# Optimization experiments

Measured on AMD Instinct MI355X. Metric: run time of the kernel, lower is better.

The kernel has to match this reference:

```python
import jax, jax.numpy as jnp
import numpy as np

BATCH, N_SEQS, SEQ_LEN, D_IN, D_OUT = 8, 4, 2048, 512, 512
LN_EPS = 1e-5


def setup_inputs() -> dict:
    key = jax.random.key(0)
    ks = jax.random.split(key, 6)
    s_in = 1.0 / np.sqrt(D_IN)
    s_out = 1.0 / np.sqrt(D_OUT)
    return {
        "x": jax.random.normal(ks[0], (BATCH, N_SEQS * SEQ_LEN * D_IN), dtype=jnp.float32),
        "Wq": jax.random.normal(ks[1], (D_OUT, D_IN), dtype=jnp.float32) * s_in,
        "Wk": jax.random.normal(ks[2], (D_OUT, D_IN), dtype=jnp.float32) * s_in,
        "Wv": jax.random.normal(ks[3], (D_OUT, D_IN), dtype=jnp.float32) * s_in,
        "Wo": jax.random.normal(ks[4], (D_OUT, D_OUT), dtype=jnp.float32) * s_out,
        "bo": jnp.zeros((D_OUT,), dtype=jnp.float32),
        "gamma": jnp.ones((D_OUT,), dtype=jnp.float32),
        "beta": jnp.zeros((D_OUT,), dtype=jnp.float32),
    }


def _phi(x):
    # positive feature map: elu(x) + 1
    return jax.nn.elu(x) + 1.0


def reference(x, Wq, Wk, Wv, Wo, bo, gamma, beta):
    batch = x.shape[0]
    xs = x.reshape(batch * N_SEQS, SEQ_LEN, D_IN)  # [B*L, S, d_in]
    Q = _phi(jnp.einsum('bsi,oi->bso', xs, Wq))     # [B*L, S, d_out]
    K = _phi(jnp.einsum('bsi,oi->bso', xs, Wk))
    V = jnp.einsum('bsi,oi->bso', xs, Wv)
    kv = jnp.einsum('bsd,bse->bde', K, V)           # [B*L, d_out, d_out]
    num = jnp.einsum('bsd,bde->bse', Q, kv)         # [B*L, S, d_out]
    k_sum = K.sum(axis=1, keepdims=True)            # [B*L, 1, d_out]
    den = jnp.maximum((Q * k_sum).sum(axis=-1, keepdims=True), 1e-6)
    out = num / den
    y = jnp.einsum('bse,oe->bso', out, Wo) + bo + out  # out_proj + residual
    mu = y.mean(axis=-1, keepdims=True)
    var = ((y - mu) ** 2).mean(axis=-1, keepdims=True)
    y = (y - mu) * jax.lax.rsqrt(var + LN_EPS) * gamma + beta
    return y.reshape(batch, -1)
```

## Files before the change

kernel.cpp:

```cpp
#include <hip/hip_runtime.h>
#include <cstdint>

typedef __bf16 bf16x8 __attribute__((ext_vector_type(8)));
typedef float  f32x4  __attribute__((ext_vector_type(4)));

#define SEQS   32
#define SLEN   2048
#define DIM    512
#define MROWS  65536

static __device__ __forceinline__ void load_lds16(const void* g, void* l) {
  __builtin_amdgcn_global_load_lds(
      (const __attribute__((address_space(1))) void*)(uintptr_t)g,
      (__attribute__((address_space(3))) void*)(uintptr_t)l,
      16, 0, 0);
}

static __device__ __forceinline__ unsigned short bfbits(float f) {
  __bf16 h = (__bf16)f;
  unsigned short u;
  __builtin_memcpy(&u, &h, 2);
  return u;
}

static __device__ __forceinline__ void gemm_core(
    const __bf16* __restrict__ A, int lda, int arow0,
    const __bf16* __restrict__ B, int ldb, int brow0,
    int K, __bf16* Asm, __bf16* Bsm, f32x4 (&acc)[4][4])
{
  const int tid  = threadIdx.x;
  const int wave = tid >> 6;
  const int lane = tid & 63;
  const int wr = wave >> 1, wc = wave & 1;
  const int lr = lane & 15, kq = lane >> 4;

  for (int kt = 0; kt < K; kt += 64) {
#pragma unroll
    for (int q = 0; q < 4; ++q) {
      const int L  = q * 4096 + tid * 16;
      const int r  = L >> 7;
      const int sl = (L >> 4) & 7;
      const int c  = ((sl ^ (r & 7)) << 3);
      load_lds16(A + (size_t)(arow0 + r) * lda + (kt + c),
                 (char*)Asm + q * 4096 + wave * 1024);
      load_lds16(B + (size_t)(brow0 + r) * ldb + (kt + c),
                 (char*)Bsm + q * 4096 + wave * 1024);
    }
    __syncthreads();

    bf16x8 af[2][4], bfr[2][4];
#pragma unroll
    for (int kk = 0; kk < 2; ++kk)
#pragma unroll
      for (int i = 0; i < 4; ++i) {
        const int rA = wr * 64 + i * 16 + lr;
        af[kk][i] = *reinterpret_cast<const bf16x8*>(
            (char*)Asm + rA * 128 + ((((kk * 4 + kq) ^ (rA & 7))) << 4));
        const int rB = wc * 64 + i * 16 + lr;
        bfr[kk][i] = *reinterpret_cast<const bf16x8*>(
            (char*)Bsm + rB * 128 + ((((kk * 4 + kq) ^ (rB & 7))) << 4));
      }
#pragma unroll
    for (int kk = 0; kk < 2; ++kk)
#pragma unroll
      for (int i = 0; i < 4; ++i)
#pragma unroll
        for (int j = 0; j < 4; ++j)
          acc[i][j] = __builtin_amdgcn_mfma_f32_16x16x32_bf16(
              af[kk][i], bfr[kk][j], acc[i][j], 0, 0, 0);
    __syncthreads();
  }
}


__global__ __launch_bounds__(256) void cast_kernel(
    const float* __restrict__ src, __bf16* __restrict__ dst, int n8)
{
  int i = blockIdx.x * blockDim.x + threadIdx.x;
  const int stride = gridDim.x * blockDim.x;
  for (; i < n8; i += stride) {
    const float4* p = reinterpret_cast<const float4*>(src + (size_t)i * 8);
    float4 a = p[0], b2 = p[1];
    float vals[8] = {a.x, a.y, a.z, a.w, b2.x, b2.y, b2.z, b2.w};
    uint32_t w[4];
#pragma unroll
    for (int t = 0; t < 4; ++t)
      w[t] = (uint32_t)bfbits(vals[2 * t]) | ((uint32_t)bfbits(vals[2 * t + 1]) << 16);
    uint4 o; o.x = w[0]; o.y = w[1]; o.z = w[2]; o.w = w[3];
    *reinterpret_cast<uint4*>(dst + (size_t)i * 8) = o;
  }
}

__global__ __launch_bounds__(256) void cast4_kernel(
    const float* __restrict__ a, const float* __restrict__ b,
    const float* __restrict__ c, const float* __restrict__ d,
    __bf16* __restrict__ ab, __bf16* __restrict__ bb,
    __bf16* __restrict__ cb, __bf16* __restrict__ db)
{
  const int z = blockIdx.y;
  const float* src = (z == 0) ? a : (z == 1) ? b : (z == 2) ? c : d;
  __bf16* dst = (z == 0) ? ab : (z == 1) ? bb : (z == 2) ? cb : db;
  const int i = blockIdx.x * 256 + threadIdx.x;
  const float4* p = reinterpret_cast<const float4*>(src + (size_t)i * 8);
  float4 x = p[0], y = p[1];
  float vals[8] = {x.x, x.y, x.z, x.w, y.x, y.y, y.z, y.w};
  uint32_t w[4];
#pragma unroll
  for (int t = 0; t < 4; ++t)
    w[t] = (uint32_t)bfbits(vals[2 * t]) | ((uint32_t)bfbits(vals[2 * t + 1]) << 16);
  uint4 o; o.x = w[0]; o.y = w[1]; o.z = w[2]; o.w = w[3];
  *reinterpret_cast<uint4*>(dst + (size_t)i * 8) = o;
}

__global__ __launch_bounds__(512, 1) void qkv_kernel(
    const __bf16* __restrict__ xb,
    const __bf16* __restrict__ Wqb, const __bf16* __restrict__ Wkb,
    const __bf16* __restrict__ Wvb,
    __bf16* __restrict__ Q, __bf16* __restrict__ KT, __bf16* __restrict__ VT,
    float* __restrict__ ksum)
{
  __shared__ __align__(16) __bf16 As[2][256 * 64];
  __shared__ __align__(16) __bf16 Bs[2][256 * 64];
  const int b = blockIdx.x;
  const int xcd = b & 7, loc = b >> 3;
  const int brow = (loc / 6) * 8 + xcd;
  const int inner = loc % 6;
  const int z = inner >> 1, bcol = inner & 1;
  const __bf16* W = (z == 0) ? Wqb : (z == 1) ? Wkb : Wvb;

  const int tid = threadIdx.x, wave = tid >> 6, lane = tid & 63;
  const int wr = wave >> 2, wn = wave & 3;
  const int lr = lane & 15, kq = lane >> 4;

  const __bf16* Abase = xb + (size_t)(brow * 256) * DIM;
  const __bf16* Bbase = W + (size_t)(bcol * 256) * DIM;

  auto stage = [&](int s, int kt) {
#pragma unroll
    for (int q = 0; q < 4; ++q) {
      const int L  = q * 8192 + tid * 16;
      const int r  = L >> 7;
      const int sl = (L >> 4) & 7;
      const int c  = ((sl ^ (r & 7)) << 3);
      load_lds16(Abase + (size_t)r * DIM + (kt + c),
                 (char*)(&As[s][0]) + q * 8192 + wave * 1024);
      load_lds16(Bbase + (size_t)r * DIM + (kt + c),
                 (char*)(&Bs[s][0]) + q * 8192 + wave * 1024);
    }
  };

  f32x4 acc[8][4] = {};

  stage(0, 0);
  __syncthreads();
  for (int t = 0; t < 8; ++t) {
    const int cur = t & 1;
    if (t < 7) stage(cur ^ 1, (t + 1) * 64);
#pragma unroll
    for (int kk = 0; kk < 2; ++kk) {
      bf16x8 bfr[4], af[8];
#pragma unroll
      for (int j = 0; j < 4; ++j) {
        const int rB = wn * 64 + j * 16 + lr;
        bfr[j] = *reinterpret_cast<const bf16x8*>(
            (const char*)(&Bs[cur][0]) + rB * 128 + (((kk * 4 + kq) ^ (rB & 7)) << 4));
      }
#pragma unroll
      for (int i = 0; i < 8; ++i) {
        const int rA = wr * 128 + i * 16 + lr;
        af[i] = *reinterpret_cast<const bf16x8*>(
            (const char*)(&As[cur][0]) + rA * 128 + (((kk * 4 + kq) ^ (rA & 7)) << 4));
      }
#pragma unroll
      for (int i = 0; i < 8; ++i)
#pragma unroll
        for (int j = 0; j < 4; ++j)
          acc[i][j] = __builtin_amdgcn_mfma_f32_16x16x32_bf16(af[i], bfr[j], acc[i][j], 0, 0, 0);
    }
    __syncthreads();
  }

  const int m00 = brow * 256 + wr * 128 + kq * 4;
  const int n00 = bcol * 256 + wn * 64 + lr;
  if (z == 0) {
#pragma unroll
    for (int i = 0; i < 8; ++i)
#pragma unroll
      for (int j = 0; j < 4; ++j) {
        const int n = n00 + j * 16;
#pragma unroll
        for (int r = 0; r < 4; ++r) {
          const int m = m00 + i * 16 + r;
          float v = acc[i][j][r];
          v = (v > 0.f) ? (v + 1.f) : __expf(v);
          Q[(size_t)m * DIM + n] = (__bf16)v;
        }
      }
  } else {
    __bf16* T = (z == 1) ? KT : VT;
    const int seq = (brow * 256) >> 11;
    float ks[4] = {0.f, 0.f, 0.f, 0.f};
#pragma unroll
    for (int i = 0; i < 8; ++i) {
      const int mb = m00 + i * 16;
      const int s0 = mb & 2047;
#pragma unroll
      for (int j = 0; j < 4; ++j) {
        const int d = n00 + j * 16;
        unsigned short h[4];
#pragma unroll
        for (int r = 0; r < 4; ++r) {
          float v = acc[i][j][r];
          if (z == 1) { v = (v > 0.f) ? (v + 1.f) : __expf(v); ks[j] += v; }
          h[r] = bfbits(v);
        }
        uint2 u;
        u.x = (uint32_t)h[0] | ((uint32_t)h[1] << 16);
        u.y = (uint32_t)h[2] | ((uint32_t)h[3] << 16);
        *reinterpret_cast<uint2*>(T + ((size_t)(seq * DIM + d) << 11) + s0) = u;
      }
    }
    if (z == 1) {
#pragma unroll
      for (int j = 0; j < 4; ++j) {
        float p = ks[j];
        p += __shfl_xor(p, 16, 64);
        p += __shfl_xor(p, 32, 64);
        if (kq == 0) atomicAdd(&ksum[seq * DIM + n00 + j * 16], p);
      }
    }
  }
}

__global__ __launch_bounds__(256) void den_kernel(
    const __bf16* __restrict__ Q, const float* __restrict__ ksum,
    float* __restrict__ den)
{
  const int lane = threadIdx.x & 63;
  const int m = blockIdx.x * 4 + (threadIdx.x >> 6);
  bf16x8 qv = *reinterpret_cast<const bf16x8*>(Q + (size_t)m * DIM + lane * 8);
  const float* kp = ksum + ((m >> 11) << 9) + lane * 8;
  float s = 0.f;
#pragma unroll
  for (int t = 0; t < 8; ++t) s += (float)qv[t] * kp[t];
#pragma unroll
  for (int off = 32; off > 0; off >>= 1) s += __shfl_xor(s, off, 64);
  if (lane == 0) den[m] = fmaxf(s, 1e-6f);
}

__global__ __launch_bounds__(256) void kv_kernel(
    const __bf16* __restrict__ VT, const __bf16* __restrict__ KT,
    __bf16* __restrict__ kvT)
{
  __shared__ __align__(16) __bf16 Asm[128 * 64];
  __shared__ __align__(16) __bf16 Bsm[128 * 64];
  const int b = blockIdx.x;
  const int xcd = b & 7, loc = b >> 3;
  const int seq = (loc >> 4) * 8 + xcd;
  const int inner = loc & 15;
  const int bxx = inner >> 2, byy = inner & 3;
  const __bf16* A = VT + (size_t)seq * DIM * SLEN;
  const __bf16* B = KT + (size_t)seq * DIM * SLEN;
  f32x4 acc[4][4] = {};
  gemm_core(A, SLEN, bxx * 128, B, SLEN, byy * 128, SLEN, Asm, Bsm, acc);

  const int tid = threadIdx.x, wave = tid >> 6, lane = tid & 63;
  const int wr = wave >> 1, wc = wave & 1, lr = lane & 15, kq = lane >> 4;
  const int m0 = bxx * 128 + wr * 64 + kq * 4;
  const int n0 = byy * 128 + wc * 64 + lr;
  __bf16* C = kvT + (size_t)seq * DIM * DIM;
#pragma unroll
  for (int i = 0; i < 4; ++i)
#pragma unroll
    for (int j = 0; j < 4; ++j)
#pragma unroll
      for (int r = 0; r < 4; ++r)
        C[(size_t)(m0 + i * 16 + r) * DIM + (n0 + j * 16)] = (__bf16)acc[i][j][r];
}

__global__ __launch_bounds__(512, 1) void num_kernel(
    const __bf16* __restrict__ Q, const __bf16* __restrict__ kvT,
    const float* __restrict__ den, __bf16* __restrict__ out)
{
  __shared__ __align__(16) __bf16 As[2][256 * 64];
  __shared__ __align__(16) __bf16 Bs[2][256 * 64];
  const int b = blockIdx.x;
  const int xcd = b & 7, loc = b >> 3;
  const int seq = (loc >> 4) * 8 + xcd;
  const int inner = loc & 15;
  const int brow = inner >> 1, bcol = inner & 1;
  const size_t grow0 = (size_t)seq * SLEN + brow * 256;

  const int tid = threadIdx.x, wave = tid >> 6, lane = tid & 63;
  const int wr = wave >> 2, wn = wave & 3;
  const int lr = lane & 15, kq = lane >> 4;

  const __bf16* Abase = Q + grow0 * DIM;
  const __bf16* Bbase = kvT + (size_t)seq * DIM * DIM + (size_t)(bcol * 256) * DIM;

  auto stage = [&](int s, int kt) {
#pragma unroll
    for (int q = 0; q < 4; ++q) {
      const int L  = q * 8192 + tid * 16;
      const int r  = L >> 7;
      const int sl = (L >> 4) & 7;
      const int c  = ((sl ^ (r & 7)) << 3);
      load_lds16(Abase + (size_t)r * DIM + (kt + c),
                 (char*)(&As[s][0]) + q * 8192 + wave * 1024);
      load_lds16(Bbase + (size_t)r * DIM + (kt + c),
                 (char*)(&Bs[s][0]) + q * 8192 + wave * 1024);
    }
  };

  f32x4 acc[8][4] = {};

  stage(0, 0);
  __syncthreads();
  for (int t = 0; t < 8; ++t) {
    const int cur = t & 1;
    if (t < 7) stage(cur ^ 1, (t + 1) * 64);
#pragma unroll
    for (int kk = 0; kk < 2; ++kk) {
      bf16x8 bfr[4], af[8];
#pragma unroll
      for (int j = 0; j < 4; ++j) {
        const int rB = wn * 64 + j * 16 + lr;
        bfr[j] = *reinterpret_cast<const bf16x8*>(
            (const char*)(&Bs[cur][0]) + rB * 128 + (((kk * 4 + kq) ^ (rB & 7)) << 4));
      }
#pragma unroll
      for (int i = 0; i < 8; ++i) {
        const int rA = wr * 128 + i * 16 + lr;
        af[i] = *reinterpret_cast<const bf16x8*>(
            (const char*)(&As[cur][0]) + rA * 128 + (((kk * 4 + kq) ^ (rA & 7)) << 4));
      }
#pragma unroll
      for (int i = 0; i < 8; ++i)
#pragma unroll
        for (int j = 0; j < 4; ++j)
          acc[i][j] = __builtin_amdgcn_mfma_f32_16x16x32_bf16(af[i], bfr[j], acc[i][j], 0, 0, 0);
    }
    __syncthreads();
  }

  const size_t g0 = grow0 + wr * 128 + kq * 4;
  const int n00 = bcol * 256 + wn * 64 + lr;
#pragma unroll
  for (int i = 0; i < 8; ++i) {
    const float4 dv = *reinterpret_cast<const float4*>(den + g0 + i * 16);
    const float rd[4] = {1.f / dv.x, 1.f / dv.y, 1.f / dv.z, 1.f / dv.w};
#pragma unroll
    for (int j = 0; j < 4; ++j)
#pragma unroll
      for (int r = 0; r < 4; ++r)
        out[(g0 + i * 16 + r) * DIM + (n00 + j * 16)] =
            (__bf16)(acc[i][j][r] * rd[r]);
  }
}

__global__ __launch_bounds__(512, 1) void final_kernel(
    const __bf16* __restrict__ outb, const __bf16* __restrict__ Wob,
    const float* __restrict__ bo, const float* __restrict__ gamma,
    const float* __restrict__ beta, float* __restrict__ y)
{
  __shared__ __align__(16) __bf16 Asm[2][128 * 32];
  __shared__ __align__(16) __bf16 Bsm[2][512 * 32];
  __shared__ float redS[4][128], redSS[4][128];
  const int tid = threadIdx.x, wave = tid >> 6, lane = tid & 63;
  const int Wr = wave >> 2, Wc = wave & 3;
  const int lr = lane & 15, kq = lane >> 4;
  const int brow = blockIdx.x;
  f32x4 acc[4][8] = {};

  auto stage = [&](int s, int kt) {
    {
      const int L = tid * 16;
      const int r = L >> 6, sl = (L >> 4) & 3;
      const int c = ((sl ^ ((r >> 1) & 3)) << 3);
      load_lds16(outb + (size_t)(brow * 128 + r) * DIM + (kt + c),
                 (char*)(&Asm[s][0]) + wave * 1024);
    }
#pragma unroll
    for (int q = 0; q < 4; ++q) {
      const int L = q * 8192 + tid * 16;
      const int r = L >> 6, sl = (L >> 4) & 3;
      const int c = ((sl ^ ((r >> 1) & 3)) << 3);
      load_lds16(Wob + (size_t)r * DIM + (kt + c),
                 (char*)(&Bsm[s][0]) + q * 8192 + wave * 1024);
    }
  };

  stage(0, 0);
  __syncthreads();
  for (int t = 0; t < 16; ++t) {
    const int cur = t & 1;
    if (t < 15) stage(cur ^ 1, (t + 1) * 32);
    bf16x8 af[4];
#pragma unroll
    for (int i = 0; i < 4; ++i) {
      const int rA = Wr * 64 + i * 16 + lr;
      af[i] = *reinterpret_cast<const bf16x8*>(
          (char*)(&Asm[cur][0]) + rA * 64 + ((kq ^ ((rA >> 1) & 3)) << 4));
    }
#pragma unroll
    for (int j = 0; j < 8; ++j) {
      const int rB = Wc * 128 + j * 16 + lr;
      bf16x8 bf = *reinterpret_cast<const bf16x8*>(
          (char*)(&Bsm[cur][0]) + rB * 64 + ((kq ^ ((rB >> 1) & 3)) << 4));
#pragma unroll
      for (int i = 0; i < 4; ++i)
        acc[i][j] = __builtin_amdgcn_mfma_f32_16x16x32_bf16(af[i], bf, acc[i][j], 0, 0, 0);
    }
    __syncthreads();
  }

  const int m0g = brow * 128;
  float sA[4][4] = {{0.f}}, ssA[4][4] = {{0.f}};
#pragma unroll
  for (int j = 0; j < 8; ++j) {
    const int n = Wc * 128 + j * 16 + lr;
    const float bon = bo[n];
#pragma unroll
    for (int i = 0; i < 4; ++i) {
      const int mb = m0g + Wr * 64 + i * 16 + kq * 4;
#pragma unroll
      for (int r = 0; r < 4; ++r) {
        float v = acc[i][j][r] + bon + (float)outb[(size_t)(mb + r) * DIM + n];
        acc[i][j][r] = v;
        sA[i][r] += v; ssA[i][r] += v * v;
      }
    }
  }
#pragma unroll
  for (int i = 0; i < 4; ++i)
#pragma unroll
    for (int r = 0; r < 4; ++r) {
      float s = sA[i][r], ss = ssA[i][r];
#pragma unroll
      for (int off = 1; off <= 8; off <<= 1) {
        s  += __shfl_xor(s,  off, 64);
        ss += __shfl_xor(ss, off, 64);
      }
      if (lr == 0) {
        const int ml = Wr * 64 + i * 16 + kq * 4 + r;
        redS[Wc][ml] = s; redSS[Wc][ml] = ss;
      }
    }
  __syncthreads();
  float mu_[4][4], rs_[4][4];
#pragma unroll
  for (int i = 0; i < 4; ++i)
#pragma unroll
    for (int r = 0; r < 4; ++r) {
      const int ml = Wr * 64 + i * 16 + kq * 4 + r;
      const float S  = redS[0][ml] + redS[1][ml] + redS[2][ml] + redS[3][ml];
      const float SS = redSS[0][ml] + redSS[1][ml] + redSS[2][ml] + redSS[3][ml];
      const float mu = S * (1.f / 512.f);
      const float var = SS * (1.f / 512.f) - mu * mu;
      mu_[i][r] = mu;
      rs_[i][r] = rsqrtf(var + 1e-5f);
    }
#pragma unroll
  for (int j = 0; j < 8; ++j) {
    const int n = Wc * 128 + j * 16 + lr;
    const float g = gamma[n], bb = beta[n];
#pragma unroll
    for (int i = 0; i < 4; ++i) {
      const int mb = m0g + Wr * 64 + i * 16 + kq * 4;
#pragma unroll
      for (int r = 0; r < 4; ++r)
        y[(size_t)(mb + r) * DIM + n] = (acc[i][j][r] - mu_[i][r]) * rs_[i][r] * g + bb;
    }
  }
}

extern "C" void kernel_launch(void* const* d_in, const int* in_sizes, int n_in,
                              void* d_out, int out_size, void* d_ws, size_t ws_size,
                              hipStream_t stream)
{
  const float* x     = (const float*)d_in[0];
  const float* Wq    = (const float*)d_in[1];
  const float* Wk    = (const float*)d_in[2];
  const float* Wv    = (const float*)d_in[3];
  const float* Wo    = (const float*)d_in[4];
  const float* bo    = (const float*)d_in[5];
  const float* gamma = (const float*)d_in[6];
  const float* beta  = (const float*)d_in[7];
  float* outp = (float*)d_out;

  char* ws = (char*)d_ws;
  const size_t SZ = 67108864;
  __bf16* xb   = (__bf16*)(ws + 0);
  __bf16* Q    = (__bf16*)(ws + SZ);
  __bf16* KT   = (__bf16*)(ws + 2 * SZ);
  __bf16* VT   = (__bf16*)(ws + 3 * SZ);
  __bf16* kvT  = (__bf16*)(ws + 4 * SZ);
  __bf16* Wqb  = (__bf16*)(ws + 4 * SZ + 16777216);
  __bf16* Wkb  = Wqb + 262144;
  __bf16* Wvb  = Wkb + 262144;
  __bf16* Wob  = Wvb + 262144;
  float*  ksum = (float*)(Wob + 262144);
  float*  den  = (float*)((char*)ksum + 65536);

  hipMemsetAsync(ksum, 0, SEQS * DIM * sizeof(float), stream);
  cast_kernel<<<4096, 256, 0, stream>>>(x, xb, MROWS * DIM / 8);
  cast4_kernel<<<dim3(128, 4), 256, 0, stream>>>(Wq, Wk, Wv, Wo, Wqb, Wkb, Wvb, Wob);

  qkv_kernel<<<1536, 512, 0, stream>>>(xb, Wqb, Wkb, Wvb, Q, KT, VT, ksum);
  den_kernel<<<16384, 256, 0, stream>>>(Q, ksum, den);
  kv_kernel<<<512, 256, 0, stream>>>(VT, KT, kvT);
  num_kernel<<<512, 512, 0, stream>>>(Q, kvT, den, xb );
  final_kernel<<<512, 512, 0, stream>>>(xb, Wob, bo, gamma, beta, outp);
}
```

Measured before the change: 393.4 us.

## Fold denominator into num GEMM via extra MFMA and merge cast kernels

Removes the separate den_kernel. The denominator Q·k_sum is now computed inside num_kernel as an extra MFMA per row tile, using k_sum staged in LDS as bf16 and broadcast as the B operand. It also merges the x cast and the four weight casts into a single grid-stride kernel, cutting two launches and one full read of Q. In exchange it adds MFMA work to the main loop, and rounding k_sum to bf16 may slightly change the denominators.

```diff
diff --git a/kernel.cpp b/kernel.cpp
--- a/kernel.cpp
+++ b/kernel.cpp
@@ -73,13 +73,28 @@
 }
 
 
-__global__ __launch_bounds__(256) void cast_kernel(
-    const float* __restrict__ src, __bf16* __restrict__ dst, int n8)
-{
+__global__ __launch_bounds__(256) void castall_kernel(
+    const float* __restrict__ x, __bf16* __restrict__ xb,
+    const float* __restrict__ wq, const float* __restrict__ wk,
+    const float* __restrict__ wv, const float* __restrict__ wo,
+    __bf16* __restrict__ wqb, __bf16* __restrict__ wkb,
+    __bf16* __restrict__ wvb, __bf16* __restrict__ wob)
+{
+  const int X8 = MROWS * DIM / 8;
+  const int W8 = DIM * DIM / 8;
+  const int total = X8 + 4 * W8;
   int i = blockIdx.x * blockDim.x + threadIdx.x;
   const int stride = gridDim.x * blockDim.x;
-  for (; i < n8; i += stride) {
-    const float4* p = reinterpret_cast<const float4*>(src + (size_t)i * 8);
+  for (; i < total; i += stride) {
+    const float* src; __bf16* dst; int off;
+    if (i < X8) { src = x; dst = xb; off = i; }
+    else {
+      const int wsel = (i - X8) / W8;
+      off = (i - X8) - wsel * W8;
+      src = (wsel == 0) ? wq : (wsel == 1) ? wk : (wsel == 2) ? wv : wo;
+      dst = (wsel == 0) ? wqb : (wsel == 1) ? wkb : (wsel == 2) ? wvb : wob;
+    }
+    const float4* p = reinterpret_cast<const float4*>(src + (size_t)off * 8);
     float4 a = p[0], b2 = p[1];
     float vals[8] = {a.x, a.y, a.z, a.w, b2.x, b2.y, b2.z, b2.w};
     uint32_t w[4];
@@ -87,29 +102,8 @@
     for (int t = 0; t < 4; ++t)
       w[t] = (uint32_t)bfbits(vals[2 * t]) | ((uint32_t)bfbits(vals[2 * t + 1]) << 16);
     uint4 o; o.x = w[0]; o.y = w[1]; o.z = w[2]; o.w = w[3];
-    *reinterpret_cast<uint4*>(dst + (size_t)i * 8) = o;
-  }
-}
-
-__global__ __launch_bounds__(256) void cast4_kernel(
-    const float* __restrict__ a, const float* __restrict__ b,
-    const float* __restrict__ c, const float* __restrict__ d,
-    __bf16* __restrict__ ab, __bf16* __restrict__ bb,
-    __bf16* __restrict__ cb, __bf16* __restrict__ db)
-{
-  const int z = blockIdx.y;
-  const float* src = (z == 0) ? a : (z == 1) ? b : (z == 2) ? c : d;
-  __bf16* dst = (z == 0) ? ab : (z == 1) ? bb : (z == 2) ? cb : db;
-  const int i = blockIdx.x * 256 + threadIdx.x;
-  const float4* p = reinterpret_cast<const float4*>(src + (size_t)i * 8);
-  float4 x = p[0], y = p[1];
-  float vals[8] = {x.x, x.y, x.z, x.w, y.x, y.y, y.z, y.w};
-  uint32_t w[4];
-#pragma unroll
-  for (int t = 0; t < 4; ++t)
-    w[t] = (uint32_t)bfbits(vals[2 * t]) | ((uint32_t)bfbits(vals[2 * t + 1]) << 16);
-  uint4 o; o.x = w[0]; o.y = w[1]; o.z = w[2]; o.w = w[3];
-  *reinterpret_cast<uint4*>(dst + (size_t)i * 8) = o;
+    *reinterpret_cast<uint4*>(dst + (size_t)off * 8) = o;
+  }
 }
 
 __global__ __launch_bounds__(512, 1) void qkv_kernel(
@@ -230,22 +224,6 @@
       }
     }
   }
-}
-
-__global__ __launch_bounds__(256) void den_kernel(
-    const __bf16* __restrict__ Q, const float* __restrict__ ksum,
-    float* __restrict__ den)
-{
-  const int lane = threadIdx.x & 63;
-  const int m = blockIdx.x * 4 + (threadIdx.x >> 6);
-  bf16x8 qv = *reinterpret_cast<const bf16x8*>(Q + (size_t)m * DIM + lane * 8);
-  const float* kp = ksum + ((m >> 11) << 9) + lane * 8;
-  float s = 0.f;
-#pragma unroll
-  for (int t = 0; t < 8; ++t) s += (float)qv[t] * kp[t];
-#pragma unroll
-  for (int off = 32; off > 0; off >>= 1) s += __shfl_xor(s, off, 64);
-  if (lane == 0) den[m] = fmaxf(s, 1e-6f);
 }
 
 __global__ __launch_bounds__(256) void kv_kernel(
@@ -280,10 +258,11 @@
 
 __global__ __launch_bounds__(512, 1) void num_kernel(
     const __bf16* __restrict__ Q, const __bf16* __restrict__ kvT,
-    const float* __restrict__ den, __bf16* __restrict__ out)
+    const float* __restrict__ ksum, __bf16* __restrict__ out)
 {
   __shared__ __align__(16) __bf16 As[2][256 * 64];
   __shared__ __align__(16) __bf16 Bs[2][256 * 64];
+  __shared__ __align__(16) __bf16 ks_lds[512];
   const int b = blockIdx.x;
   const int xcd = b & 7, loc = b >> 3;
   const int seq = (loc >> 4) * 8 + xcd;
@@ -313,7 +292,9 @@
   };
 
   f32x4 acc[8][4] = {};
-
+  f32x4 accd[8] = {};
+
+  ks_lds[tid] = (__bf16)ksum[seq * DIM + tid];
   stage(0, 0);
   __syncthreads();
   for (int t = 0; t < 8; ++t) {
@@ -322,6 +303,8 @@
 #pragma unroll
     for (int kk = 0; kk < 2; ++kk) {
       bf16x8 bfr[4], af[8];
+      const bf16x8 ksf = *reinterpret_cast<const bf16x8*>(
+          &ks_lds[t * 64 + kk * 32 + kq * 8]);
 #pragma unroll
       for (int j = 0; j < 4; ++j) {
         const int rB = wn * 64 + j * 16 + lr;
@@ -335,10 +318,12 @@
             (const char*)(&As[cur][0]) + rA * 128 + (((kk * 4 + kq) ^ (rA & 7)) << 4));
       }
 #pragma unroll
-      for (int i = 0; i < 8; ++i)
+      for (int i = 0; i < 8; ++i) {
 #pragma unroll
         for (int j = 0; j < 4; ++j)
           acc[i][j] = __builtin_amdgcn_mfma_f32_16x16x32_bf16(af[i], bfr[j], acc[i][j], 0, 0, 0);
+        accd[i] = __builtin_amdgcn_mfma_f32_16x16x32_bf16(af[i], ksf, accd[i], 0, 0, 0);
+      }
     }
     __syncthreads();
   }
@@ -347,8 +332,10 @@
   const int n00 = bcol * 256 + wn * 64 + lr;
 #pragma unroll
   for (int i = 0; i < 8; ++i) {
-    const float4 dv = *reinterpret_cast<const float4*>(den + g0 + i * 16);
-    const float rd[4] = {1.f / dv.x, 1.f / dv.y, 1.f / dv.z, 1.f / dv.w};
+    float rd[4];
+#pragma unroll
+    for (int r = 0; r < 4; ++r)
+      rd[r] = 1.f / fmaxf(accd[i][r], 1e-6f);
 #pragma unroll
     for (int j = 0; j < 4; ++j)
 #pragma unroll
@@ -500,15 +487,13 @@
   __bf16* Wvb  = Wkb + 262144;
   __bf16* Wob  = Wvb + 262144;
   float*  ksum = (float*)(Wob + 262144);
-  float*  den  = (float*)((char*)ksum + 65536);
 
   hipMemsetAsync(ksum, 0, SEQS * DIM * sizeof(float), stream);
-  cast_kernel<<<4096, 256, 0, stream>>>(x, xb, MROWS * DIM / 8);
-  cast4_kernel<<<dim3(128, 4), 256, 0, stream>>>(Wq, Wk, Wv, Wo, Wqb, Wkb, Wvb, Wob);
+  castall_kernel<<<4224, 256, 0, stream>>>(x, xb, Wq, Wk, Wv, Wo,
+                                           Wqb, Wkb, Wvb, Wob);
 
   qkv_kernel<<<1536, 512, 0, stream>>>(xb, Wqb, Wkb, Wvb, Q, KT, VT, ksum);
-  den_kernel<<<16384, 256, 0, stream>>>(Q, ksum, den);
   kv_kernel<<<512, 256, 0, stream>>>(VT, KT, kvT);
-  num_kernel<<<512, 512, 0, stream>>>(Q, kvT, den, xb );
+  num_kernel<<<512, 512, 0, stream>>>(Q, kvT, ksum, xb );
   final_kernel<<<512, 512, 0, stream>>>(xb, Wob, bo, gamma, beta, outp);
 }
```

Measured after the change: 375.1 us. 4.6% less time.
